# Optimization experiments

Hardware: AMD Instinct MI355X
Metric: run time of the kernel (lower is better)

## Reference

```python
import jax, jax.numpy as jnp
import numpy as np

B, H, W = 4, 64, 1024
h, w = 32, 512
K = 16
C = 64
EPS = 1e-5


def setup_inputs() -> dict:
    key = jax.random.key(0)
    ks = jax.random.split(key, 8)
    n_sampled = h * w
    xyz_proj = jax.random.normal(ks[0], (B, H, W, 3), dtype=jnp.float32)
    points_proj = jax.random.normal(ks[1], (B, H, W, C), dtype=jnp.float32)
    xyz_sampled_proj = jax.random.normal(ks[2], (B, h, w, 3), dtype=jnp.float32)
    # Precomputed neighbor selection (stand-in for fused_conv_random_k, which is
    # a non-differentiable custom CUDA op producing detached indices + mask).
    neighbor_idx = jax.random.randint(ks[3], (B, n_sampled * K), 0, H * W, dtype=jnp.int32)
    valid_mask = (jax.random.uniform(ks[4], (B, n_sampled, K, 1)) > 0.1).astype(jnp.float32)
    # 1x1 conv MLP params (torch Conv2d weight (out,in,1,1) stored here as (in,out))
    def mk(k, cin, cout):
        kw, = jax.random.split(k, 1)
        wgt = jax.random.normal(kw, (cin, cout), dtype=jnp.float32) * (1.0 / np.sqrt(cin))
        return wgt
    w0 = mk(ks[5], 3 + C, 64)
    w1 = mk(ks[6], 64, 64)
    w2 = mk(ks[7], 64, 128)
    z = lambda c: jnp.zeros((c,), jnp.float32)
    o = lambda c: jnp.ones((c,), jnp.float32)
    return dict(
        xyz_proj=xyz_proj, points_proj=points_proj, xyz_sampled_proj=xyz_sampled_proj,
        neighbor_idx=neighbor_idx, valid_mask=valid_mask,
        w0=w0, b0=z(64), g0=o(64), be0=z(64), m0=z(64), v0=o(64),
        w1=w1, b1=z(64), g1=o(64), be1=z(64), m1=z(64), v1=o(64),
        w2=w2, b2=z(128), g2=o(128), be2=z(128), m2=z(128), v2=o(128),
    )


def _conv_bn_relu(x, wgt, b, g, be, m, v):
    # 1x1 conv == matmul over channel dim; BN in eval mode with running stats.
    y = jnp.einsum('bnkc,co->bnko', x, wgt) + b
    y = g * (y - m) * jax.lax.rsqrt(v + EPS) + be
    return jax.nn.relu(y)


def reference(xyz_proj, points_proj, xyz_sampled_proj, neighbor_idx, valid_mask,
              w0, b0, g0, be0, m0, v0,
              w1, b1, g1, be1, m1, v1,
              w2, b2, g2, be2, m2, v2):
    Bc = xyz_proj.shape[0]
    Cc = points_proj.shape[3]
    hh, ww = xyz_sampled_proj.shape[1], xyz_sampled_proj.shape[2]
    n_sampled = hh * ww
    xyz_bn3 = xyz_proj.reshape(Bc, -1, 3)          # (B, H*W, 3)
    points_bnc = points_proj.reshape(Bc, -1, Cc)   # (B, H*W, C)
    idx = neighbor_idx[..., None]                  # (B, n*K, 1)
    new_xyz_group = jnp.take_along_axis(xyz_bn3, idx, axis=1).reshape(Bc, n_sampled, K, 3)
    new_points_group = jnp.take_along_axis(points_bnc, idx, axis=1).reshape(Bc, n_sampled, K, Cc)
    new_xyz_group = new_xyz_group * valid_mask
    new_points_group = new_points_group * valid_mask
    new_xyz = xyz_sampled_proj.reshape(Bc, n_sampled, 1, 3)
    xyz_diff = new_xyz_group - new_xyz             # broadcast over K
    feat = jnp.concatenate([xyz_diff, new_points_group], axis=-1)  # (B, n, K, 3+C)
    feat = _conv_bn_relu(feat, w0, b0, g0, be0, m0, v0)
    feat = _conv_bn_relu(feat, w1, b1, g1, be1, m1, v1)
    feat = _conv_bn_relu(feat, w2, b2, g2, be2, m2, v2)
    points_down_sample = jnp.max(feat, axis=2)     # (B, n, 128) max-pool over K
    points_down_sample_proj = points_down_sample.reshape(Bc, hh, ww, -1)
    return points_down_sample, points_down_sample_proj
```

## Files before the change

kernel.cpp:

```cpp
#include <hip/hip_runtime.h>


#define NGRP_    8192
#define OUTHALF_ 8388608
#define WS_      72
#define XS2_     36
#define EPS_     1e-5f
#define GRID_    768

typedef _Float16 h8    __attribute__((ext_vector_type(8)));
typedef float    f32x4 __attribute__((ext_vector_type(4)));
typedef unsigned u32x2 __attribute__((ext_vector_type(2)));

__global__ __launch_bounds__(256) void cvt_pts_kernel(
    const float* __restrict__ src, _Float16* __restrict__ dst)
{
    const size_t i = ((size_t)blockIdx.x * 256 + threadIdx.x) * 8;
    f32x4 a = *(const f32x4*)(src + i);
    f32x4 b = *(const f32x4*)(src + i + 4);
    h8 o;
#pragma unroll
    for (int j = 0; j < 4; ++j) { o[j] = (_Float16)a[j]; o[4 + j] = (_Float16)b[j]; }
    *(h8*)(dst + i) = o;
}

#define PK(lo, hi) ({                                                          \
    const _Float16 _l = (_Float16)fmaxf((lo), 0.f);                            \
    const _Float16 _h = (_Float16)fmaxf((hi), 0.f);                            \
    (unsigned)__builtin_bit_cast(unsigned short, _l) |                         \
    ((unsigned)__builtin_bit_cast(unsigned short, _h) << 16); })

template<bool PRE>
__global__ __launch_bounds__(256, 3) void pnsa_main(
    const float* __restrict__ xyz,
    const void*  __restrict__ ptsv,
    const float* __restrict__ xyzs,
    const int*   __restrict__ nidx,
    const float* __restrict__ vmask,
    const float* __restrict__ w0, const float* __restrict__ b0,
    const float* __restrict__ g0, const float* __restrict__ be0,
    const float* __restrict__ m0, const float* __restrict__ v0,
    const float* __restrict__ w1, const float* __restrict__ b1,
    const float* __restrict__ g1, const float* __restrict__ be1,
    const float* __restrict__ m1, const float* __restrict__ v1,
    const float* __restrict__ w2, const float* __restrict__ b2,
    const float* __restrict__ g2, const float* __restrict__ be2,
    const float* __restrict__ m2, const float* __restrict__ v2,
    float*       __restrict__ out)
{
    __shared__ __align__(16) _Float16 ldsW1[64 * WS_];
    __shared__ __align__(16) _Float16 ldsW2[128 * WS_];
    __shared__ __align__(16) float    s1sh[64], t1sh[64];
    __shared__ __align__(16) float    s2sh[128], t2sh[128];
    __shared__ __align__(16) unsigned ldsX[4][2][16 * XS2_];

    const int tid  = threadIdx.x;
    const int wave = tid >> 6;
    const int lane = tid & 63;
    const int l15  = lane & 15;
    const int quad = lane >> 4;

    unsigned* XA = &ldsX[wave][0][0];
    unsigned* XB = &ldsX[wave][1][0];

    if (tid < 64) {
        const float s = g1[tid] * rsqrtf(v1[tid] + EPS_);
        s1sh[tid] = s;
        t1sh[tid] = (b1[tid] - m1[tid]) * s + be1[tid];
    }
    if (tid < 128) {
        const float s = g2[tid] * rsqrtf(v2[tid] + EPS_);
        s2sh[tid] = s;
        t2sh[tid] = (b2[tid] - m2[tid]) * s + be2[tid];
    }
    __syncthreads();
    for (int idx = tid; idx < 64 * 64; idx += 256) {
        const int k = idx >> 6, n = idx & 63;
        ldsW1[n * WS_ + k] = (_Float16)(w1[idx] * s1sh[n]);
    }
    for (int idx = tid; idx < 64 * 128; idx += 256) {
        const int k = idx >> 7, n = idx & 127;
        ldsW2[n * WS_ + k] = (_Float16)(w2[idx] * s2sh[n]);
    }
    __syncthreads();

    h8 b0f[4][3];
#pragma unroll
    for (int nt = 0; nt < 4; ++nt) {
        const int ch = nt * 16 + l15;
        const float s = g0[ch] * rsqrtf(v0[ch] + EPS_);
        const float t0 = (b0[ch] - m0[ch]) * s + be0[ch];
#pragma unroll
        for (int kk = 0; kk < 3; ++kk) {
            h8 f;
#pragma unroll
            for (int j = 0; j < 8; ++j) {
                const int k = kk * 32 + quad * 8 + j;
                float wv = 0.f;
                if (k < 64)       wv = w0[(3 + k) * 64 + ch] * s;
                else if (k < 67)  wv = w0[(k - 64) * 64 + ch] * s;
                else if (k == 67) wv = t0;
                f[j] = (_Float16)wv;
            }
            b0f[nt][kk] = f;
        }
    }

    const int g0i = blockIdx.x;
    const int pA0 = (g0i << 3) + (wave << 1);
    int nbA = nidx[(pA0 << 4) + l15];
    int nbB = nidx[((pA0 + 1) << 4) + l15];

    for (int grp = g0i; grp < NGRP_; grp += GRID_) {
        const int pA = (grp << 3) + (wave << 1);
        const int pB = pA + 1;
        const int gn = (grp + GRID_ < NGRP_) ? grp + GRID_ : grp;
        const int pAn = (gn << 3) + (wave << 1);

        const size_t rowA = (size_t)(((pA >> 14) << 16) + nbA);
        const size_t rowB = (size_t)(((pB >> 14) << 16) + nbB);
        h8 qA0, qA1, qB0, qB1;
        if constexpr (PRE) {
            const _Float16* pwA = (const _Float16*)ptsv + (rowA << 6);
            const _Float16* pwB = (const _Float16*)ptsv + (rowB << 6);
            qA0 = *(const h8*)(pwA + quad * 8);
            qA1 = *(const h8*)(pwA + 32 + quad * 8);
            qB0 = *(const h8*)(pwB + quad * 8);
            qB1 = *(const h8*)(pwB + 32 + quad * 8);
        } else {
            const float* pwA = (const float*)ptsv + (rowA << 6);
            const float* pwB = (const float*)ptsv + (rowB << 6);
            f32x4 r0, r1, r2, r3;
            r0 = *(const f32x4*)(pwA + quad * 8);      r1 = *(const f32x4*)(pwA + quad * 8 + 4);
            r2 = *(const f32x4*)(pwA + 32 + quad * 8); r3 = *(const f32x4*)(pwA + 32 + quad * 8 + 4);
#pragma unroll
            for (int j = 0; j < 4; ++j) { qA0[j]=(_Float16)r0[j]; qA0[4+j]=(_Float16)r1[j];
                                          qA1[j]=(_Float16)r2[j]; qA1[4+j]=(_Float16)r3[j]; }
            r0 = *(const f32x4*)(pwB + quad * 8);      r1 = *(const f32x4*)(pwB + quad * 8 + 4);
            r2 = *(const f32x4*)(pwB + 32 + quad * 8); r3 = *(const f32x4*)(pwB + 32 + quad * 8 + 4);
#pragma unroll
            for (int j = 0; j < 4; ++j) { qB0[j]=(_Float16)r0[j]; qB0[4+j]=(_Float16)r1[j];
                                          qB1[j]=(_Float16)r2[j]; qB1[4+j]=(_Float16)r3[j]; }
        }
        const float mkA = vmask[(pA << 4) + l15];
        const float mkB = vmask[(pB << 4) + l15];
        const float* xgA = xyz + rowA * 3;
        const float* xgB = xyz + rowB * 3;
        const float xgA0 = xgA[0], xgA1 = xgA[1], xgA2 = xgA[2];
        const float xgB0 = xgB[0], xgB1 = xgB[1], xgB2 = xgB[2];
        const float* xsA = xyzs + (size_t)pA * 3;
        const float* xsB = xyzs + (size_t)pB * 3;
        const float xsA0 = xsA[0], xsA1 = xsA[1], xsA2 = xsA[2];
        const float xsB0 = xsB[0], xsB1 = xsB[1], xsB2 = xsB[2];

        const int nbAn = nidx[(pAn << 4) + l15];
        const int nbBn = nidx[((pAn + 1) << 4) + l15];

        if (mkA == 0.0f) { qA0 = (h8)(_Float16)0.f; qA1 = (h8)(_Float16)0.f; }
        if (mkB == 0.0f) { qB0 = (h8)(_Float16)0.f; qB1 = (h8)(_Float16)0.f; }
        h8 aA2 = (h8)(_Float16)0.f, aB2 = (h8)(_Float16)0.f;
        if (quad == 0) {
            aA2[0] = (_Float16)(xgA0 * mkA - xsA0);
            aA2[1] = (_Float16)(xgA1 * mkA - xsA1);
            aA2[2] = (_Float16)(xgA2 * mkA - xsA2);
            aA2[3] = (_Float16)1.0f;
            aB2[0] = (_Float16)(xgB0 * mkB - xsB0);
            aB2[1] = (_Float16)(xgB1 * mkB - xsB1);
            aB2[2] = (_Float16)(xgB2 * mkB - xsB2);
            aB2[3] = (_Float16)1.0f;
        }

#pragma unroll
        for (int nt = 0; nt < 4; ++nt) {
            f32x4 aA = {0.f,0.f,0.f,0.f}, aB = {0.f,0.f,0.f,0.f};
            aA = __builtin_amdgcn_mfma_f32_16x16x32_f16(b0f[nt][0], qA0, aA, 0, 0, 0);
            aA = __builtin_amdgcn_mfma_f32_16x16x32_f16(b0f[nt][1], qA1, aA, 0, 0, 0);
            aA = __builtin_amdgcn_mfma_f32_16x16x32_f16(b0f[nt][2], aA2, aA, 0, 0, 0);
            aB = __builtin_amdgcn_mfma_f32_16x16x32_f16(b0f[nt][0], qB0, aB, 0, 0, 0);
            aB = __builtin_amdgcn_mfma_f32_16x16x32_f16(b0f[nt][1], qB1, aB, 0, 0, 0);
            aB = __builtin_amdgcn_mfma_f32_16x16x32_f16(b0f[nt][2], aB2, aB, 0, 0, 0);
            u32x2 pkA = {PK(aA[0], aA[1]), PK(aA[2], aA[3])};
            u32x2 pkB = {PK(aB[0], aB[1]), PK(aB[2], aB[3])};
            *(u32x2*)(XA + l15 * XS2_ + nt * 8 + quad * 2) = pkA;
            *(u32x2*)(XB + l15 * XS2_ + nt * 8 + quad * 2) = pkB;
        }

        h8 xA0 = *(const h8*)(XA + l15 * XS2_ + quad * 4);
        h8 xA1 = *(const h8*)(XA + l15 * XS2_ + 16 + quad * 4);
        h8 xB0 = *(const h8*)(XB + l15 * XS2_ + quad * 4);
        h8 xB1 = *(const h8*)(XB + l15 * XS2_ + 16 + quad * 4);
#pragma unroll 2
        for (int nt = 0; nt < 4; ++nt) {
            const _Float16* wrow = ldsW1 + (nt * 16 + l15) * WS_ + quad * 8;
            h8 wa = *(const h8*)(wrow);
            h8 wb = *(const h8*)(wrow + 32);
            const f32x4 t1 = *(const f32x4*)(t1sh + nt * 16 + quad * 4);
            f32x4 aA = t1, aB = t1;
            aA = __builtin_amdgcn_mfma_f32_16x16x32_f16(wa, xA0, aA, 0, 0, 0);
            aA = __builtin_amdgcn_mfma_f32_16x16x32_f16(wb, xA1, aA, 0, 0, 0);
            aB = __builtin_amdgcn_mfma_f32_16x16x32_f16(wa, xB0, aB, 0, 0, 0);
            aB = __builtin_amdgcn_mfma_f32_16x16x32_f16(wb, xB1, aB, 0, 0, 0);
            u32x2 pkA = {PK(aA[0], aA[1]), PK(aA[2], aA[3])};
            u32x2 pkB = {PK(aB[0], aB[1]), PK(aB[2], aB[3])};
            *(u32x2*)(XA + l15 * XS2_ + nt * 8 + quad * 2) = pkA;
            *(u32x2*)(XB + l15 * XS2_ + nt * 8 + quad * 2) = pkB;
        }

        h8 yA0 = *(const h8*)(XA + l15 * XS2_ + quad * 4);
        h8 yA1 = *(const h8*)(XA + l15 * XS2_ + 16 + quad * 4);
        h8 yB0 = *(const h8*)(XB + l15 * XS2_ + quad * 4);
        h8 yB1 = *(const h8*)(XB + l15 * XS2_ + 16 + quad * 4);
        float* obA = out + ((size_t)pA << 7);
        float* obB = out + ((size_t)pB << 7);
#pragma unroll 2
        for (int nt = 0; nt < 8; ++nt) {
            const _Float16* wrow = ldsW2 + (nt * 16 + l15) * WS_ + quad * 8;
            h8 wa = *(const h8*)(wrow);
            h8 wb = *(const h8*)(wrow + 32);
            const float t2 = t2sh[nt * 16 + l15];
            f32x4 aA = {0.f,0.f,0.f,0.f}, aB = {0.f,0.f,0.f,0.f};
            aA = __builtin_amdgcn_mfma_f32_16x16x32_f16(yA0, wa, aA, 0, 0, 0);
            aA = __builtin_amdgcn_mfma_f32_16x16x32_f16(yA1, wb, aA, 0, 0, 0);
            aB = __builtin_amdgcn_mfma_f32_16x16x32_f16(yB0, wa, aB, 0, 0, 0);
            aB = __builtin_amdgcn_mfma_f32_16x16x32_f16(yB1, wb, aB, 0, 0, 0);
            float vA = fmaxf(fmaxf(aA[0], aA[1]), fmaxf(aA[2], aA[3])) + t2;
            float vB = fmaxf(fmaxf(aB[0], aB[1]), fmaxf(aB[2], aB[3])) + t2;
            vA = fmaxf(vA, 0.f);  vB = fmaxf(vB, 0.f);
            vA = fmaxf(vA, __shfl_xor(vA, 16, 64));
            vA = fmaxf(vA, __shfl_xor(vA, 32, 64));
            vB = fmaxf(vB, __shfl_xor(vB, 16, 64));
            vB = fmaxf(vB, __shfl_xor(vB, 32, 64));
            if (quad == 0) {
                obA[nt * 16 + l15]            = vA;
                obA[OUTHALF_ + nt * 16 + l15] = vA;
                obB[nt * 16 + l15]            = vB;
                obB[OUTHALF_ + nt * 16 + l15] = vB;
            }
        }

        nbA = nbAn; nbB = nbBn;
    }
}

extern "C" void kernel_launch(void* const* d_in, const int* in_sizes, int n_in,
                              void* d_out, int out_size, void* d_ws, size_t ws_size,
                              hipStream_t stream) {
    const float* xyz   = (const float*)d_in[0];
    const float* pts   = (const float*)d_in[1];
    const float* xyzs  = (const float*)d_in[2];
    const int*   nidx  = (const int*)d_in[3];
    const float* vmask = (const float*)d_in[4];
    const float *w0 = (const float*)d_in[5],  *b0 = (const float*)d_in[6],
                *g0 = (const float*)d_in[7],  *be0 = (const float*)d_in[8],
                *m0 = (const float*)d_in[9],  *v0 = (const float*)d_in[10];
    const float *w1 = (const float*)d_in[11], *b1 = (const float*)d_in[12],
                *g1 = (const float*)d_in[13], *be1 = (const float*)d_in[14],
                *m1 = (const float*)d_in[15], *v1 = (const float*)d_in[16];
    const float *w2 = (const float*)d_in[17], *b2 = (const float*)d_in[18],
                *g2 = (const float*)d_in[19], *be2 = (const float*)d_in[20],
                *m2 = (const float*)d_in[21], *v2 = (const float*)d_in[22];
    float* outp = (float*)d_out;

    const size_t PTS_ELEMS = 16777216ull;
    if (ws_size >= PTS_ELEMS * sizeof(_Float16)) {
        _Float16* ptsh = (_Float16*)d_ws;
        cvt_pts_kernel<<<dim3(8192), dim3(256), 0, stream>>>(pts, ptsh);
        pnsa_main<true><<<dim3(GRID_), dim3(256), 0, stream>>>(
            xyz, (const void*)ptsh, xyzs, nidx, vmask,
            w0, b0, g0, be0, m0, v0,
            w1, b1, g1, be1, m1, v1,
            w2, b2, g2, be2, m2, v2, outp);
    } else {
        pnsa_main<false><<<dim3(GRID_), dim3(256), 0, stream>>>(
            xyz, (const void*)pts, xyzs, nidx, vmask,
            w0, b0, g0, be0, m0, v0,
            w1, b1, g1, be1, m1, v1,
            w2, b2, g2, be2, m2, v2, outp);
    }
}
```

Measured before the change: 226.2 us.

## Process one point per wave with software-pipelined gather prefetch and higher occupancy

Each wave now handles a single sampled point per iteration instead of two, and the gathered point features, xyz, mask and sampled xyz for the next iteration are loaded one iteration ahead so gather latency overlaps the MFMA chain. The LDS scratch is halved, the scale arrays are dropped (scales recomputed inline), one barrier is removed, and launch bounds go from 3 to 4 blocks per CU with a larger grid. This costs more registers for the prefetched values and gives less ILP per wave, relying on occupancy to hide latency instead.

```diff
diff --git a/kernel.cpp b/kernel.cpp
--- a/kernel.cpp
+++ b/kernel.cpp
@@ -1,12 +1,12 @@
 #include <hip/hip_runtime.h>
 
 
-#define NGRP_    8192
+#define NGRP_    16384
 #define OUTHALF_ 8388608
 #define WS_      72
 #define XS2_     36
 #define EPS_     1e-5f
-#define GRID_    768
+#define GRID_    1024
 
 typedef _Float16 h8    __attribute__((ext_vector_type(8)));
 typedef float    f32x4 __attribute__((ext_vector_type(4)));
@@ -31,7 +31,27 @@
     ((unsigned)__builtin_bit_cast(unsigned short, _h) << 16); })
 
 template<bool PRE>
-__global__ __launch_bounds__(256, 3) void pnsa_main(
+__device__ __forceinline__ void load_pt(const void* __restrict__ ptsv,
+                                        size_t row, int quad, h8& o0, h8& o1)
+{
+    if constexpr (PRE) {
+        const _Float16* pw = (const _Float16*)ptsv + (row << 6);
+        o0 = *(const h8*)(pw + quad * 8);
+        o1 = *(const h8*)(pw + 32 + quad * 8);
+    } else {
+        const float* pw = (const float*)ptsv + (row << 6);
+        f32x4 r0 = *(const f32x4*)(pw + quad * 8);
+        f32x4 r1 = *(const f32x4*)(pw + quad * 8 + 4);
+        f32x4 r2 = *(const f32x4*)(pw + 32 + quad * 8);
+        f32x4 r3 = *(const f32x4*)(pw + 32 + quad * 8 + 4);
+#pragma unroll
+        for (int j = 0; j < 4; ++j) { o0[j]=(_Float16)r0[j]; o0[4+j]=(_Float16)r1[j];
+                                      o1[j]=(_Float16)r2[j]; o1[4+j]=(_Float16)r3[j]; }
+    }
+}
+
+template<bool PRE>
+__global__ __launch_bounds__(256, 4) void pnsa_main(
     const float* __restrict__ xyz,
     const void*  __restrict__ ptsv,
     const float* __restrict__ xyzs,
@@ -50,9 +70,9 @@
 {
     __shared__ __align__(16) _Float16 ldsW1[64 * WS_];
     __shared__ __align__(16) _Float16 ldsW2[128 * WS_];
-    __shared__ __align__(16) float    s1sh[64], t1sh[64];
-    __shared__ __align__(16) float    s2sh[128], t2sh[128];
-    __shared__ __align__(16) unsigned ldsX[4][2][16 * XS2_];
+    __shared__ __align__(16) float    t1sh[64];
+    __shared__ __align__(16) float    t2sh[128];
+    __shared__ __align__(16) unsigned ldsX[4][16 * XS2_];
 
     const int tid  = threadIdx.x;
     const int wave = tid >> 6;
@@ -60,27 +80,23 @@
     const int l15  = lane & 15;
     const int quad = lane >> 4;
 
-    unsigned* XA = &ldsX[wave][0][0];
-    unsigned* XB = &ldsX[wave][1][0];
+    unsigned* Xp = &ldsX[wave][0];
 
     if (tid < 64) {
         const float s = g1[tid] * rsqrtf(v1[tid] + EPS_);
-        s1sh[tid] = s;
         t1sh[tid] = (b1[tid] - m1[tid]) * s + be1[tid];
     }
     if (tid < 128) {
         const float s = g2[tid] * rsqrtf(v2[tid] + EPS_);
-        s2sh[tid] = s;
         t2sh[tid] = (b2[tid] - m2[tid]) * s + be2[tid];
     }
-    __syncthreads();
     for (int idx = tid; idx < 64 * 64; idx += 256) {
         const int k = idx >> 6, n = idx & 63;
-        ldsW1[n * WS_ + k] = (_Float16)(w1[idx] * s1sh[n]);
+        ldsW1[n * WS_ + k] = (_Float16)(w1[idx] * (g1[n] * rsqrtf(v1[n] + EPS_)));
     }
     for (int idx = tid; idx < 64 * 128; idx += 256) {
         const int k = idx >> 7, n = idx & 127;
-        ldsW2[n * WS_ + k] = (_Float16)(w2[idx] * s2sh[n]);
+        ldsW2[n * WS_ + k] = (_Float16)(w2[idx] * (g2[n] * rsqrtf(v2[n] + EPS_)));
     }
     __syncthreads();
 
@@ -106,139 +122,100 @@
         }
     }
 
-    const int g0i = blockIdx.x;
-    const int pA0 = (g0i << 3) + (wave << 1);
-    int nbA = nidx[(pA0 << 4) + l15];
-    int nbB = nidx[((pA0 + 1) << 4) + l15];
-
-    for (int grp = g0i; grp < NGRP_; grp += GRID_) {
-        const int pA = (grp << 3) + (wave << 1);
-        const int pB = pA + 1;
-        const int gn = (grp + GRID_ < NGRP_) ? grp + GRID_ : grp;
-        const int pAn = (gn << 3) + (wave << 1);
-
-        const size_t rowA = (size_t)(((pA >> 14) << 16) + nbA);
-        const size_t rowB = (size_t)(((pB >> 14) << 16) + nbB);
-        h8 qA0, qA1, qB0, qB1;
-        if constexpr (PRE) {
-            const _Float16* pwA = (const _Float16*)ptsv + (rowA << 6);
-            const _Float16* pwB = (const _Float16*)ptsv + (rowB << 6);
-            qA0 = *(const h8*)(pwA + quad * 8);
-            qA1 = *(const h8*)(pwA + 32 + quad * 8);
-            qB0 = *(const h8*)(pwB + quad * 8);
-            qB1 = *(const h8*)(pwB + 32 + quad * 8);
-        } else {
-            const float* pwA = (const float*)ptsv + (rowA << 6);
-            const float* pwB = (const float*)ptsv + (rowB << 6);
-            f32x4 r0, r1, r2, r3;
-            r0 = *(const f32x4*)(pwA + quad * 8);      r1 = *(const f32x4*)(pwA + quad * 8 + 4);
-            r2 = *(const f32x4*)(pwA + 32 + quad * 8); r3 = *(const f32x4*)(pwA + 32 + quad * 8 + 4);
-#pragma unroll
-            for (int j = 0; j < 4; ++j) { qA0[j]=(_Float16)r0[j]; qA0[4+j]=(_Float16)r1[j];
-                                          qA1[j]=(_Float16)r2[j]; qA1[4+j]=(_Float16)r3[j]; }
-            r0 = *(const f32x4*)(pwB + quad * 8);      r1 = *(const f32x4*)(pwB + quad * 8 + 4);
-            r2 = *(const f32x4*)(pwB + 32 + quad * 8); r3 = *(const f32x4*)(pwB + 32 + quad * 8 + 4);
-#pragma unroll
-            for (int j = 0; j < 4; ++j) { qB0[j]=(_Float16)r0[j]; qB0[4+j]=(_Float16)r1[j];
-                                          qB1[j]=(_Float16)r2[j]; qB1[4+j]=(_Float16)r3[j]; }
-        }
-        const float mkA = vmask[(pA << 4) + l15];
-        const float mkB = vmask[(pB << 4) + l15];
-        const float* xgA = xyz + rowA * 3;
-        const float* xgB = xyz + rowB * 3;
-        const float xgA0 = xgA[0], xgA1 = xgA[1], xgA2 = xgA[2];
-        const float xgB0 = xgB[0], xgB1 = xgB[1], xgB2 = xgB[2];
-        const float* xsA = xyzs + (size_t)pA * 3;
-        const float* xsB = xyzs + (size_t)pB * 3;
-        const float xsA0 = xsA[0], xsA1 = xsA[1], xsA2 = xsA[2];
-        const float xsB0 = xsB[0], xsB1 = xsB[1], xsB2 = xsB[2];
-
-        const int nbAn = nidx[(pAn << 4) + l15];
-        const int nbBn = nidx[((pAn + 1) << 4) + l15];
-
-        if (mkA == 0.0f) { qA0 = (h8)(_Float16)0.f; qA1 = (h8)(_Float16)0.f; }
-        if (mkB == 0.0f) { qB0 = (h8)(_Float16)0.f; qB1 = (h8)(_Float16)0.f; }
-        h8 aA2 = (h8)(_Float16)0.f, aB2 = (h8)(_Float16)0.f;
+    h8 q0, q1;
+    float xg0, xg1, xg2, xs0, xs1, xs2, mk;
+    int nb_nxt;
+    {
+        const int p = (blockIdx.x << 2) + wave;
+        const int nb0 = nidx[(p << 4) + l15];
+        const size_t row = (size_t)(((p >> 14) << 16) + nb0);
+        load_pt<PRE>(ptsv, row, quad, q0, q1);
+        const float* xgp = xyz + row * 3;
+        xg0 = xgp[0]; xg1 = xgp[1]; xg2 = xgp[2];
+        mk = vmask[(p << 4) + l15];
+        const float* xsp = xyzs + (size_t)p * 3;
+        xs0 = xsp[0]; xs1 = xsp[1]; xs2 = xsp[2];
+        const int g1i = (blockIdx.x + GRID_ < NGRP_) ? blockIdx.x + GRID_ : blockIdx.x;
+        nb_nxt = nidx[(((g1i << 2) + wave) << 4) + l15];
+    }
+
+    for (int grp = blockIdx.x; grp < NGRP_; grp += GRID_) {
+        const int p = (grp << 2) + wave;
+        const int gn  = (grp + GRID_ < NGRP_) ? grp + GRID_ : grp;
+        const int gnn = (gn + GRID_ < NGRP_) ? gn + GRID_ : gn;
+        const int pn  = (gn << 2) + wave;
+
+        const size_t rowN = (size_t)(((pn >> 14) << 16) + nb_nxt);
+        h8 q0n, q1n;
+        load_pt<PRE>(ptsv, rowN, quad, q0n, q1n);
+        const float* xgpn = xyz + rowN * 3;
+        const float xg0n = xgpn[0], xg1n = xgpn[1], xg2n = xgpn[2];
+        const float mkn = vmask[(pn << 4) + l15];
+        const float* xspn = xyzs + (size_t)pn * 3;
+        const float xs0n = xspn[0], xs1n = xspn[1], xs2n = xspn[2];
+        const int nb_n2 = nidx[(((gnn << 2) + wave) << 4) + l15];
+
+        h8 a0 = q0, a1 = q1;
+        if (mk == 0.0f) { a0 = (h8)(_Float16)0.f; a1 = (h8)(_Float16)0.f; }
+        h8 a2 = (h8)(_Float16)0.f;
         if (quad == 0) {
-            aA2[0] = (_Float16)(xgA0 * mkA - xsA0);
-            aA2[1] = (_Float16)(xgA1 * mkA - xsA1);
-            aA2[2] = (_Float16)(xgA2 * mkA - xsA2);
-            aA2[3] = (_Float16)1.0f;
-            aB2[0] = (_Float16)(xgB0 * mkB - xsB0);
-            aB2[1] = (_Float16)(xgB1 * mkB - xsB1);
-            aB2[2] = (_Float16)(xgB2 * mkB - xsB2);
-            aB2[3] = (_Float16)1.0f;
+            a2[0] = (_Float16)(xg0 * mk - xs0);
+            a2[1] = (_Float16)(xg1 * mk - xs1);
+            a2[2] = (_Float16)(xg2 * mk - xs2);
+            a2[3] = (_Float16)1.0f;
         }
 
 #pragma unroll
         for (int nt = 0; nt < 4; ++nt) {
-            f32x4 aA = {0.f,0.f,0.f,0.f}, aB = {0.f,0.f,0.f,0.f};
-            aA = __builtin_amdgcn_mfma_f32_16x16x32_f16(b0f[nt][0], qA0, aA, 0, 0, 0);
-            aA = __builtin_amdgcn_mfma_f32_16x16x32_f16(b0f[nt][1], qA1, aA, 0, 0, 0);
-            aA = __builtin_amdgcn_mfma_f32_16x16x32_f16(b0f[nt][2], aA2, aA, 0, 0, 0);
-            aB = __builtin_amdgcn_mfma_f32_16x16x32_f16(b0f[nt][0], qB0, aB, 0, 0, 0);
-            aB = __builtin_amdgcn_mfma_f32_16x16x32_f16(b0f[nt][1], qB1, aB, 0, 0, 0);
-            aB = __builtin_amdgcn_mfma_f32_16x16x32_f16(b0f[nt][2], aB2, aB, 0, 0, 0);
-            u32x2 pkA = {PK(aA[0], aA[1]), PK(aA[2], aA[3])};
-            u32x2 pkB = {PK(aB[0], aB[1]), PK(aB[2], aB[3])};
-            *(u32x2*)(XA + l15 * XS2_ + nt * 8 + quad * 2) = pkA;
-            *(u32x2*)(XB + l15 * XS2_ + nt * 8 + quad * 2) = pkB;
-        }
-
-        h8 xA0 = *(const h8*)(XA + l15 * XS2_ + quad * 4);
-        h8 xA1 = *(const h8*)(XA + l15 * XS2_ + 16 + quad * 4);
-        h8 xB0 = *(const h8*)(XB + l15 * XS2_ + quad * 4);
-        h8 xB1 = *(const h8*)(XB + l15 * XS2_ + 16 + quad * 4);
+            f32x4 acc = {0.f, 0.f, 0.f, 0.f};
+            acc = __builtin_amdgcn_mfma_f32_16x16x32_f16(b0f[nt][0], a0, acc, 0, 0, 0);
+            acc = __builtin_amdgcn_mfma_f32_16x16x32_f16(b0f[nt][1], a1, acc, 0, 0, 0);
+            acc = __builtin_amdgcn_mfma_f32_16x16x32_f16(b0f[nt][2], a2, acc, 0, 0, 0);
+            u32x2 pk = {PK(acc[0], acc[1]), PK(acc[2], acc[3])};
+            *(u32x2*)(Xp + l15 * XS2_ + nt * 8 + quad * 2) = pk;
+        }
+
+        h8 x0 = *(const h8*)(Xp + l15 * XS2_ + quad * 4);
+        h8 x1 = *(const h8*)(Xp + l15 * XS2_ + 16 + quad * 4);
 #pragma unroll 2
         for (int nt = 0; nt < 4; ++nt) {
             const _Float16* wrow = ldsW1 + (nt * 16 + l15) * WS_ + quad * 8;
             h8 wa = *(const h8*)(wrow);
             h8 wb = *(const h8*)(wrow + 32);
             const f32x4 t1 = *(const f32x4*)(t1sh + nt * 16 + quad * 4);
-            f32x4 aA = t1, aB = t1;
-            aA = __builtin_amdgcn_mfma_f32_16x16x32_f16(wa, xA0, aA, 0, 0, 0);
-            aA = __builtin_amdgcn_mfma_f32_16x16x32_f16(wb, xA1, aA, 0, 0, 0);
-            aB = __builtin_amdgcn_mfma_f32_16x16x32_f16(wa, xB0, aB, 0, 0, 0);
-            aB = __builtin_amdgcn_mfma_f32_16x16x32_f16(wb, xB1, aB, 0, 0, 0);
-            u32x2 pkA = {PK(aA[0], aA[1]), PK(aA[2], aA[3])};
-            u32x2 pkB = {PK(aB[0], aB[1]), PK(aB[2], aB[3])};
-            *(u32x2*)(XA + l15 * XS2_ + nt * 8 + quad * 2) = pkA;
-            *(u32x2*)(XB + l15 * XS2_ + nt * 8 + quad * 2) = pkB;
-        }
-
-        h8 yA0 = *(const h8*)(XA + l15 * XS2_ + quad * 4);
-        h8 yA1 = *(const h8*)(XA + l15 * XS2_ + 16 + quad * 4);
-        h8 yB0 = *(const h8*)(XB + l15 * XS2_ + quad * 4);
-        h8 yB1 = *(const h8*)(XB + l15 * XS2_ + 16 + quad * 4);
-        float* obA = out + ((size_t)pA << 7);
-        float* obB = out + ((size_t)pB << 7);
+            f32x4 acc = t1;
+            acc = __builtin_amdgcn_mfma_f32_16x16x32_f16(wa, x0, acc, 0, 0, 0);
+            acc = __builtin_amdgcn_mfma_f32_16x16x32_f16(wb, x1, acc, 0, 0, 0);
+            u32x2 pk = {PK(acc[0], acc[1]), PK(acc[2], acc[3])};
+            *(u32x2*)(Xp + l15 * XS2_ + nt * 8 + quad * 2) = pk;
+        }
+
+        h8 y0 = *(const h8*)(Xp + l15 * XS2_ + quad * 4);
+        h8 y1 = *(const h8*)(Xp + l15 * XS2_ + 16 + quad * 4);
+        float* ob = out + ((size_t)p << 7);
 #pragma unroll 2
         for (int nt = 0; nt < 8; ++nt) {
             const _Float16* wrow = ldsW2 + (nt * 16 + l15) * WS_ + quad * 8;
             h8 wa = *(const h8*)(wrow);
             h8 wb = *(const h8*)(wrow + 32);
             const float t2 = t2sh[nt * 16 + l15];
-            f32x4 aA = {0.f,0.f,0.f,0.f}, aB = {0.f,0.f,0.f,0.f};
-            aA = __builtin_amdgcn_mfma_f32_16x16x32_f16(yA0, wa, aA, 0, 0, 0);
-            aA = __builtin_amdgcn_mfma_f32_16x16x32_f16(yA1, wb, aA, 0, 0, 0);
-            aB = __builtin_amdgcn_mfma_f32_16x16x32_f16(yB0, wa, aB, 0, 0, 0);
-            aB = __builtin_amdgcn_mfma_f32_16x16x32_f16(yB1, wb, aB, 0, 0, 0);
-            float vA = fmaxf(fmaxf(aA[0], aA[1]), fmaxf(aA[2], aA[3])) + t2;
-            float vB = fmaxf(fmaxf(aB[0], aB[1]), fmaxf(aB[2], aB[3])) + t2;
-            vA = fmaxf(vA, 0.f);  vB = fmaxf(vB, 0.f);
-            vA = fmaxf(vA, __shfl_xor(vA, 16, 64));
-            vA = fmaxf(vA, __shfl_xor(vA, 32, 64));
-            vB = fmaxf(vB, __shfl_xor(vB, 16, 64));
-            vB = fmaxf(vB, __shfl_xor(vB, 32, 64));
+            f32x4 acc = {0.f, 0.f, 0.f, 0.f};
+            acc = __builtin_amdgcn_mfma_f32_16x16x32_f16(y0, wa, acc, 0, 0, 0);
+            acc = __builtin_amdgcn_mfma_f32_16x16x32_f16(y1, wb, acc, 0, 0, 0);
+            float v = fmaxf(fmaxf(acc[0], acc[1]), fmaxf(acc[2], acc[3])) + t2;
+            v = fmaxf(v, 0.f);
+            v = fmaxf(v, __shfl_xor(v, 16, 64));
+            v = fmaxf(v, __shfl_xor(v, 32, 64));
             if (quad == 0) {
-                obA[nt * 16 + l15]            = vA;
-                obA[OUTHALF_ + nt * 16 + l15] = vA;
-                obB[nt * 16 + l15]            = vB;
-                obB[OUTHALF_ + nt * 16 + l15] = vB;
+                ob[nt * 16 + l15]            = v;
+                ob[OUTHALF_ + nt * 16 + l15] = v;
             }
         }
 
-        nbA = nbAn; nbB = nbBn;
+        q0 = q0n; q1 = q1n;
+        xg0 = xg0n; xg1 = xg1n; xg2 = xg2n;
+        xs0 = xs0n; xs1 = xs1n; xs2 = xs2n;
+        mk = mkn; nb_nxt = nb_n2;
     }
 }
 
```

Measured after the change: 227.6 us. No clear change (+0.6%).

## Software-pipeline neighbor gathers one iteration ahead and partition groups per XCD

Applied to the files above, without the earlier changes.

The gathered point features, xyz, mask and sampled xyz for the next iteration are now loaded before the current iteration's MFMA work, and neighbor indices are prefetched two iterations ahead. This hides the latency of the random gathers behind the compute. Work is also split so each XCD (blockIdx & 7) processes a contiguous range of 1024 groups with 96 blocks per XCD, which should improve L2 locality of the gathered rows. In exchange the kernel holds more live registers, which may reduce occupancy under launch_bounds(256,3) or cause spills.

```diff
diff --git a/kernel.cpp b/kernel.cpp
--- a/kernel.cpp
+++ b/kernel.cpp
@@ -2,6 +2,8 @@
 
 
 #define NGRP_    8192
+#define GPX_     1024
+#define BPX_     96
 #define OUTHALF_ 8388608
 #define WS_      72
 #define XS2_     36
@@ -29,6 +31,43 @@
     const _Float16 _h = (_Float16)fmaxf((hi), 0.f);                            \
     (unsigned)__builtin_bit_cast(unsigned short, _l) |                         \
     ((unsigned)__builtin_bit_cast(unsigned short, _h) << 16); })
+
+struct PtData {
+    h8 q0, q1;
+    float xg0, xg1, xg2;
+    float xs0, xs1, xs2;
+    float mk;
+};
+
+template<bool PRE>
+__device__ __forceinline__ PtData load_point(
+    const void* __restrict__ ptsv, const float* __restrict__ xyz,
+    const float* __restrict__ xyzs, const float* __restrict__ vmask,
+    int p, int nb, int quad, int l15)
+{
+    PtData d;
+    const size_t row = (size_t)(((p >> 14) << 16) + nb);
+    if constexpr (PRE) {
+        const _Float16* pw = (const _Float16*)ptsv + (row << 6);
+        d.q0 = *(const h8*)(pw + quad * 8);
+        d.q1 = *(const h8*)(pw + 32 + quad * 8);
+    } else {
+        const float* pw = (const float*)ptsv + (row << 6);
+        f32x4 r0 = *(const f32x4*)(pw + quad * 8);
+        f32x4 r1 = *(const f32x4*)(pw + quad * 8 + 4);
+        f32x4 r2 = *(const f32x4*)(pw + 32 + quad * 8);
+        f32x4 r3 = *(const f32x4*)(pw + 32 + quad * 8 + 4);
+#pragma unroll
+        for (int j = 0; j < 4; ++j) { d.q0[j]=(_Float16)r0[j]; d.q0[4+j]=(_Float16)r1[j];
+                                      d.q1[j]=(_Float16)r2[j]; d.q1[4+j]=(_Float16)r3[j]; }
+    }
+    const float* xgp = xyz + row * 3;
+    d.xg0 = xgp[0]; d.xg1 = xgp[1]; d.xg2 = xgp[2];
+    d.mk = vmask[(p << 4) + l15];
+    const float* xsp = xyzs + (size_t)p * 3;
+    d.xs0 = xsp[0]; d.xs1 = xsp[1]; d.xs2 = xsp[2];
+    return d;
+}
 
 template<bool PRE>
 __global__ __launch_bounds__(256, 3) void pnsa_main(
@@ -106,67 +145,51 @@
         }
     }
 
-    const int g0i = blockIdx.x;
-    const int pA0 = (g0i << 3) + (wave << 1);
-    int nbA = nidx[(pA0 << 4) + l15];
-    int nbB = nidx[((pA0 + 1) << 4) + l15];
-
-    for (int grp = g0i; grp < NGRP_; grp += GRID_) {
+    const int xcd = blockIdx.x & 7;
+    const int bix = blockIdx.x >> 3;
+    const int gbase = xcd * GPX_;
+
+    PtData dA, dB;
+    int nbA_nxt, nbB_nxt;
+    {
+        const int grp0 = gbase + bix;
+        const int pA0 = (grp0 << 3) + (wave << 1);
+        const int nbA0 = nidx[(pA0 << 4) + l15];
+        const int nbB0 = nidx[((pA0 + 1) << 4) + l15];
+        dA = load_point<PRE>(ptsv, xyz, xyzs, vmask, pA0,     nbA0, quad, l15);
+        dB = load_point<PRE>(ptsv, xyz, xyzs, vmask, pA0 + 1, nbB0, quad, l15);
+        const int g1i = (bix + BPX_ < GPX_) ? bix + BPX_ : bix;
+        const int pA1 = ((gbase + g1i) << 3) + (wave << 1);
+        nbA_nxt = nidx[(pA1 << 4) + l15];
+        nbB_nxt = nidx[((pA1 + 1) << 4) + l15];
+    }
+
+    for (int g = bix; g < GPX_; g += BPX_) {
+        const int grp = gbase + g;
         const int pA = (grp << 3) + (wave << 1);
         const int pB = pA + 1;
-        const int gn = (grp + GRID_ < NGRP_) ? grp + GRID_ : grp;
-        const int pAn = (gn << 3) + (wave << 1);
-
-        const size_t rowA = (size_t)(((pA >> 14) << 16) + nbA);
-        const size_t rowB = (size_t)(((pB >> 14) << 16) + nbB);
-        h8 qA0, qA1, qB0, qB1;
-        if constexpr (PRE) {
-            const _Float16* pwA = (const _Float16*)ptsv + (rowA << 6);
-            const _Float16* pwB = (const _Float16*)ptsv + (rowB << 6);
-            qA0 = *(const h8*)(pwA + quad * 8);
-            qA1 = *(const h8*)(pwA + 32 + quad * 8);
-            qB0 = *(const h8*)(pwB + quad * 8);
-            qB1 = *(const h8*)(pwB + 32 + quad * 8);
-        } else {
-            const float* pwA = (const float*)ptsv + (rowA << 6);
-            const float* pwB = (const float*)ptsv + (rowB << 6);
-            f32x4 r0, r1, r2, r3;
-            r0 = *(const f32x4*)(pwA + quad * 8);      r1 = *(const f32x4*)(pwA + quad * 8 + 4);
-            r2 = *(const f32x4*)(pwA + 32 + quad * 8); r3 = *(const f32x4*)(pwA + 32 + quad * 8 + 4);
-#pragma unroll
-            for (int j = 0; j < 4; ++j) { qA0[j]=(_Float16)r0[j]; qA0[4+j]=(_Float16)r1[j];
-                                          qA1[j]=(_Float16)r2[j]; qA1[4+j]=(_Float16)r3[j]; }
-            r0 = *(const f32x4*)(pwB + quad * 8);      r1 = *(const f32x4*)(pwB + quad * 8 + 4);
-            r2 = *(const f32x4*)(pwB + 32 + quad * 8); r3 = *(const f32x4*)(pwB + 32 + quad * 8 + 4);
-#pragma unroll
-            for (int j = 0; j < 4; ++j) { qB0[j]=(_Float16)r0[j]; qB0[4+j]=(_Float16)r1[j];
-                                          qB1[j]=(_Float16)r2[j]; qB1[4+j]=(_Float16)r3[j]; }
-        }
-        const float mkA = vmask[(pA << 4) + l15];
-        const float mkB = vmask[(pB << 4) + l15];
-        const float* xgA = xyz + rowA * 3;
-        const float* xgB = xyz + rowB * 3;
-        const float xgA0 = xgA[0], xgA1 = xgA[1], xgA2 = xgA[2];
-        const float xgB0 = xgB[0], xgB1 = xgB[1], xgB2 = xgB[2];
-        const float* xsA = xyzs + (size_t)pA * 3;
-        const float* xsB = xyzs + (size_t)pB * 3;
-        const float xsA0 = xsA[0], xsA1 = xsA[1], xsA2 = xsA[2];
-        const float xsB0 = xsB[0], xsB1 = xsB[1], xsB2 = xsB[2];
-
-        const int nbAn = nidx[(pAn << 4) + l15];
-        const int nbBn = nidx[((pAn + 1) << 4) + l15];
-
-        if (mkA == 0.0f) { qA0 = (h8)(_Float16)0.f; qA1 = (h8)(_Float16)0.f; }
-        if (mkB == 0.0f) { qB0 = (h8)(_Float16)0.f; qB1 = (h8)(_Float16)0.f; }
+        const int gn  = (g + BPX_ < GPX_) ? g + BPX_ : g;
+        const int gnn = (gn + BPX_ < GPX_) ? gn + BPX_ : gn;
+        const int pAn = ((gbase + gn) << 3) + (wave << 1);
+        const int pA2 = ((gbase + gnn) << 3) + (wave << 1);
+
+        PtData dAn = load_point<PRE>(ptsv, xyz, xyzs, vmask, pAn,     nbA_nxt, quad, l15);
+        PtData dBn = load_point<PRE>(ptsv, xyz, xyzs, vmask, pAn + 1, nbB_nxt, quad, l15);
+        const int nbA_n2 = nidx[(pA2 << 4) + l15];
+        const int nbB_n2 = nidx[((pA2 + 1) << 4) + l15];
+
+        h8 qA0 = dA.q0, qA1 = dA.q1, qB0 = dB.q0, qB1 = dB.q1;
+        if (dA.mk == 0.0f) { qA0 = (h8)(_Float16)0.f; qA1 = (h8)(_Float16)0.f; }
+        if (dB.mk == 0.0f) { qB0 = (h8)(_Float16)0.f; qB1 = (h8)(_Float16)0.f; }
         h8 aA2 = (h8)(_Float16)0.f, aB2 = (h8)(_Float16)0.f;
         if (quad == 0) {
-            aA2[0] = (_Float16)(xgA0 * mkA - xsA0);
-            aA2[1] = (_Float16)(xgA1 * mkA - xsA1);
-            aA2[2] = (_Float16)(xgA2 * mkA - xsA2);
+            aA2[0] = (_Float16)(dA.xg0 * dA.mk - dA.xs0);
+            aA2[1] = (_Float16)(dA.xg1 * dA.mk - dA.xs1);
+            aA2[2] = (_Float16)(dA.xg2 * dA.mk - dA.xs2);
             aA2[3] = (_Float16)1.0f;
-            aB2[0] = (_Float16)(xgB0 * mkB - xsB0);
-            aB2[1] = (_Float16)(xgB1 * mkB - xsB1);
-            aB2[2] = (_Float16)(xgB2 * mkB - xsB2);
+            aB2[0] = (_Float16)(dB.xg0 * dB.mk - dB.xs0);
+            aB2[1] = (_Float16)(dB.xg1 * dB.mk - dB.xs1);
+            aB2[2] = (_Float16)(dB.xg2 * dB.mk - dB.xs2);
             aB2[3] = (_Float16)1.0f;
         }
 
@@ -238,7 +261,8 @@
             }
         }
 
-        nbA = nbAn; nbB = nbBn;
+        dA = dAn; dB = dBn;
+        nbA_nxt = nbA_n2; nbB_nxt = nbB_n2;
     }
 }
 
```

After: 222.9 us. About the same (-1.4%).
